# Kernel tuning notes

Measured on AMD Instinct MI355X. Metric: run time of the kernel, lower is better.

The kernel has to match this reference:

```python
import jax, jax.numpy as jnp
import numpy as np


def setup_inputs() -> dict:
    key = jax.random.key(0)
    k1, k2 = jax.random.split(key)
    B, T, D = 32, 2048, 1024
    query = jax.random.normal(k1, (B, D), dtype=jnp.float32)
    values = jax.random.normal(k2, (B, T, D), dtype=jnp.float32)
    return {"query": query, "values": values}


def reference(query, values):
    # score[b,t] = sum_d query[b,d] * values[b,t,d]
    score = jnp.einsum("bd,btd->bt", query, values)[..., None]  # [B,T,1]
    attention_weights = jax.nn.softmax(score, axis=1)           # [B,T,1]
    # context[b,d] = sum_t w[b,t] * values[b,t,d]
    context_vector = jnp.einsum("bt,btd->bd", attention_weights[..., 0], values)
    return (context_vector, attention_weights)
```

## Files before the change

kernel.cpp:

```cpp
#include <hip/hip_runtime.h>
#include <hip/hip_bf16.h>

#define BB 32
#define TT 2048
#define DD 1024
#define TCHUNK 32
#define NC (TT / TCHUNK)
#define WPB 4
#define BLOCKS_PER_B (NC / WPB)


__global__ __launch_bounds__(256) void attn_pass1(
    const float* __restrict__ query,
    const float* __restrict__ values,
    float* __restrict__ ws) {
    float* scores = ws;
    float* pm = ws + BB * TT;
    float* pl = pm + BB * NC;
    float* pctx = pl + BB * NC;

    const int tid  = threadIdx.x;
    const int lane = tid & 63;
    const int wave = tid >> 6;
    const int b     = blockIdx.x / BLOCKS_PER_B;
    const int chunk = (blockIdx.x % BLOCKS_PER_B) * WPB + wave;
    const int t0    = chunk * TCHUNK;

    const float4* qrow = (const float4*)(query + (size_t)b * DD);
    float qf[16];
#pragma unroll
    for (int g = 0; g < 4; g++) {
        float4 q4 = qrow[g * 64 + lane];
        qf[4 * g + 0] = q4.x; qf[4 * g + 1] = q4.y;
        qf[4 * g + 2] = q4.z; qf[4 * g + 3] = q4.w;
    }

    const float4* vbase = (const float4*)(values + ((size_t)b * TT + t0) * DD);

    float m = -INFINITY, l = 0.f;
    float ctx[16];
#pragma unroll
    for (int k = 0; k < 16; k++) ctx[k] = 0.f;

    float4 cur0[4], cur1[4];
#pragma unroll
    for (int g = 0; g < 4; g++) {
        cur0[g] = vbase[g * 64 + lane];
        cur1[g] = vbase[256 + g * 64 + lane];
    }

    for (int r = 0; r < TCHUNK; r += 2) {
        float4 nxt0[4], nxt1[4];
        const bool have_next = (r + 2 < TCHUNK);
        if (have_next) {
#pragma unroll
            for (int g = 0; g < 4; g++) {
                nxt0[g] = vbase[(size_t)(r + 2) * 256 + g * 64 + lane];
                nxt1[g] = vbase[(size_t)(r + 3) * 256 + g * 64 + lane];
            }
        }
        float vf0[16], vf1[16];
#pragma unroll
        for (int g = 0; g < 4; g++) {
            vf0[4 * g + 0] = cur0[g].x; vf0[4 * g + 1] = cur0[g].y;
            vf0[4 * g + 2] = cur0[g].z; vf0[4 * g + 3] = cur0[g].w;
            vf1[4 * g + 0] = cur1[g].x; vf1[4 * g + 1] = cur1[g].y;
            vf1[4 * g + 2] = cur1[g].z; vf1[4 * g + 3] = cur1[g].w;
        }

        float s0 = 0.f, s1 = 0.f;
#pragma unroll
        for (int k = 0; k < 16; k++) {
            s0 = fmaf(qf[k], vf0[k], s0);
            s1 = fmaf(qf[k], vf1[k], s1);
        }
#pragma unroll
        for (int off = 32; off >= 1; off >>= 1) {
            s0 += __shfl_xor(s0, off, 64);
            s1 += __shfl_xor(s1, off, 64);
        }

        if (s0 <= m) {
            float p = __expf(s0 - m);
            l += p;
#pragma unroll
            for (int k = 0; k < 16; k++) ctx[k] = fmaf(p, vf0[k], ctx[k]);
        } else {
            float corr = __expf(m - s0);
            m = s0;
            l = fmaf(l, corr, 1.f);
#pragma unroll
            for (int k = 0; k < 16; k++) ctx[k] = fmaf(ctx[k], corr, vf0[k]);
        }
        if (s1 <= m) {
            float p = __expf(s1 - m);
            l += p;
#pragma unroll
            for (int k = 0; k < 16; k++) ctx[k] = fmaf(p, vf1[k], ctx[k]);
        } else {
            float corr = __expf(m - s1);
            m = s1;
            l = fmaf(l, corr, 1.f);
#pragma unroll
            for (int k = 0; k < 16; k++) ctx[k] = fmaf(ctx[k], corr, vf1[k]);
        }

        if (lane == 0) {
            float2* sp = (float2*)(scores + (size_t)b * TT + t0 + r);
            *sp = make_float2(s0, s1);
        }
        if (have_next) {
#pragma unroll
            for (int g = 0; g < 4; g++) { cur0[g] = nxt0[g]; cur1[g] = nxt1[g]; }
        }
    }

    const int ci = b * NC + chunk;
    if (lane == 0) { pm[ci] = m; pl[ci] = l; }
    float4* pc = (float4*)(pctx + (size_t)ci * DD);
#pragma unroll
    for (int g = 0; g < 4; g++)
        pc[g * 64 + lane] = make_float4(ctx[4 * g + 0], ctx[4 * g + 1],
                                        ctx[4 * g + 2], ctx[4 * g + 3]);
}

__global__ __launch_bounds__(256) void attn_pass2(
    const float* __restrict__ ws,
    float* __restrict__ out) {
    const float* scores = ws;
    const float* pm = ws + BB * TT;
    const float* pl = pm + BB * NC;
    const float* pctx = pl + BB * NC;

    const int tid   = threadIdx.x;
    const int b     = blockIdx.x >> 2;
    const int slice = blockIdx.x & 3;

    __shared__ float s_e[NC];
    __shared__ float s_M, s_L;
    if (tid < 64) {
        float mi = pm[b * NC + tid];
        float li = pl[b * NC + tid];
        float M = mi;
#pragma unroll
        for (int off = 32; off >= 1; off >>= 1) M = fmaxf(M, __shfl_xor(M, off, 64));
        float e  = __expf(mi - M);
        float lw = li * e;
#pragma unroll
        for (int off = 32; off >= 1; off >>= 1) lw += __shfl_xor(lw, off, 64);
        s_e[tid] = e;
        if (tid == 0) { s_M = M; s_L = lw; }
    }
    __syncthreads();
    const float M  = s_M;
    const float rL = 1.0f / s_L;

    const int d = slice * 256 + tid;
    const float* base = pctx + (size_t)b * NC * DD + d;
    float acc = 0.f;
#pragma unroll 8
    for (int i = 0; i < NC; i++) acc = fmaf(base[(size_t)i * DD], s_e[i], acc);
    out[(size_t)b * DD + d] = acc * rL;

    float* wout = out + BB * DD;
#pragma unroll
    for (int k = 0; k < 2; k++) {
        int t = slice * 512 + k * 256 + tid;
        float w = __expf(scores[(size_t)b * TT + t] - M) * rL;
        wout[(size_t)b * TT + t] = w;
    }
}

extern "C" void kernel_launch(void* const* d_in, const int* in_sizes, int n_in,
                              void* d_out, int out_size, void* d_ws, size_t ws_size,
                              hipStream_t stream) {
    const float* query  = (const float*)d_in[0];
    const float* values = (const float*)d_in[1];
    float* ws = (float*)d_ws;
    float* out = (float*)d_out;

    attn_pass1<<<dim3(BB * BLOCKS_PER_B), dim3(256), 0, stream>>>(query, values, ws);
    attn_pass2<<<dim3(BB * 4), dim3(256), 0, stream>>>(ws, out);
}
```

Measured before the change: 367.7 us.

## Fuse softmax combine pass into main kernel via last-block atomic counter

Each block first merges its four waves' partial max, sum and context in LDS, so it writes one partial per block instead of one per wave. The second kernel is removed; the last block to finish each batch row, found with an atomic counter, does the final cross-block reduction and writes the normalized weights. This removes one kernel launch and cuts partial-context traffic by four. In exchange it adds a memset launch, thread fences, 16KB of LDS per block, and a serial tail done by 32 single blocks.

```diff
diff --git a/kernel.cpp b/kernel.cpp
--- a/kernel.cpp
+++ b/kernel.cpp
@@ -8,22 +8,30 @@
 #define NC (TT / TCHUNK)
 #define WPB 4
 #define BLOCKS_PER_B (NC / WPB)
-
-
-__global__ __launch_bounds__(256) void attn_pass1(
+#define NBLK BLOCKS_PER_B
+
+#define WS_PM   (BB * TT)
+#define WS_PL   (WS_PM + BB * NBLK)
+#define WS_PCTX (WS_PL + BB * NBLK)
+#define WS_CNT  (WS_PCTX + BB * NBLK * DD)
+
+__global__ __launch_bounds__(256) void attn_fused(
     const float* __restrict__ query,
     const float* __restrict__ values,
-    float* __restrict__ ws) {
+    float* __restrict__ ws,
+    float* __restrict__ out) {
     float* scores = ws;
-    float* pm = ws + BB * TT;
-    float* pl = pm + BB * NC;
-    float* pctx = pl + BB * NC;
+    float* pm   = ws + WS_PM;
+    float* pl   = ws + WS_PL;
+    float* pctx = ws + WS_PCTX;
+    int*   cnt  = (int*)(ws + WS_CNT);
 
     const int tid  = threadIdx.x;
     const int lane = tid & 63;
     const int wave = tid >> 6;
     const int b     = blockIdx.x / BLOCKS_PER_B;
-    const int chunk = (blockIdx.x % BLOCKS_PER_B) * WPB + wave;
+    const int blkin = blockIdx.x % BLOCKS_PER_B;
+    const int chunk = blkin * WPB + wave;
     const int t0    = chunk * TCHUNK;
 
     const float4* qrow = (const float4*)(query + (size_t)b * DD);
@@ -115,59 +123,84 @@
         }
     }
 
-    const int ci = b * NC + chunk;
-    if (lane == 0) { pm[ci] = m; pl[ci] = l; }
-    float4* pc = (float4*)(pctx + (size_t)ci * DD);
+    __shared__ float lds_ctx[WPB][DD];
+    __shared__ float lds_m[WPB], lds_l[WPB];
+    __shared__ int   s_last;
+
+    float4* lw = (float4*)lds_ctx[wave];
 #pragma unroll
     for (int g = 0; g < 4; g++)
-        pc[g * 64 + lane] = make_float4(ctx[4 * g + 0], ctx[4 * g + 1],
+        lw[g * 64 + lane] = make_float4(ctx[4 * g + 0], ctx[4 * g + 1],
                                         ctx[4 * g + 2], ctx[4 * g + 3]);
-}
-
-__global__ __launch_bounds__(256) void attn_pass2(
-    const float* __restrict__ ws,
-    float* __restrict__ out) {
-    const float* scores = ws;
-    const float* pm = ws + BB * TT;
-    const float* pl = pm + BB * NC;
-    const float* pctx = pl + BB * NC;
-
-    const int tid   = threadIdx.x;
-    const int b     = blockIdx.x >> 2;
-    const int slice = blockIdx.x & 3;
-
-    __shared__ float s_e[NC];
-    __shared__ float s_M, s_L;
+    if (lane == 0) { lds_m[wave] = m; lds_l[wave] = l; }
+    __syncthreads();
+
+    const float m0 = lds_m[0], m1 = lds_m[1], m2 = lds_m[2], m3 = lds_m[3];
+    const float mB = fmaxf(fmaxf(m0, m1), fmaxf(m2, m3));
+    const float e0 = __expf(m0 - mB), e1 = __expf(m1 - mB);
+    const float e2 = __expf(m2 - mB), e3 = __expf(m3 - mB);
+    const float lB = lds_l[0] * e0 + lds_l[1] * e1 + lds_l[2] * e2 + lds_l[3] * e3;
+
+    const int bc = b * NBLK + blkin;
+    {
+        float4 a = ((const float4*)lds_ctx[0])[tid];
+        float4 c = ((const float4*)lds_ctx[1])[tid];
+        float4 d = ((const float4*)lds_ctx[2])[tid];
+        float4 e = ((const float4*)lds_ctx[3])[tid];
+        float4 o;
+        o.x = fmaf(a.x, e0, fmaf(c.x, e1, fmaf(d.x, e2, e.x * e3)));
+        o.y = fmaf(a.y, e0, fmaf(c.y, e1, fmaf(d.y, e2, e.y * e3)));
+        o.z = fmaf(a.z, e0, fmaf(c.z, e1, fmaf(d.z, e2, e.z * e3)));
+        o.w = fmaf(a.w, e0, fmaf(c.w, e1, fmaf(d.w, e2, e.w * e3)));
+        ((float4*)(pctx + (size_t)bc * DD))[tid] = o;
+    }
+    if (tid == 0) { pm[bc] = mB; pl[bc] = lB; }
+
+    __threadfence();
+    __syncthreads();
+    if (tid == 0) s_last = (atomicAdd(&cnt[b], 1) == NBLK - 1);
+    __syncthreads();
+    if (!s_last) return;
+    __threadfence();
+
+    __shared__ float s_e16[NBLK];
+    __shared__ float s_M, s_rL;
     if (tid < 64) {
-        float mi = pm[b * NC + tid];
-        float li = pl[b * NC + tid];
+        float mi = (tid < NBLK) ? pm[b * NBLK + tid] : -INFINITY;
+        float li = (tid < NBLK) ? pl[b * NBLK + tid] : 0.f;
         float M = mi;
 #pragma unroll
         for (int off = 32; off >= 1; off >>= 1) M = fmaxf(M, __shfl_xor(M, off, 64));
         float e  = __expf(mi - M);
-        float lw = li * e;
-#pragma unroll
-        for (int off = 32; off >= 1; off >>= 1) lw += __shfl_xor(lw, off, 64);
-        s_e[tid] = e;
-        if (tid == 0) { s_M = M; s_L = lw; }
+        float lw2 = li * e;
+#pragma unroll
+        for (int off = 32; off >= 1; off >>= 1) lw2 += __shfl_xor(lw2, off, 64);
+        if (tid < NBLK) s_e16[tid] = e;
+        if (tid == 0) { s_M = M; s_rL = 1.0f / lw2; }
     }
     __syncthreads();
     const float M  = s_M;
-    const float rL = 1.0f / s_L;
-
-    const int d = slice * 256 + tid;
-    const float* base = pctx + (size_t)b * NC * DD + d;
-    float acc = 0.f;
-#pragma unroll 8
-    for (int i = 0; i < NC; i++) acc = fmaf(base[(size_t)i * DD], s_e[i], acc);
-    out[(size_t)b * DD + d] = acc * rL;
+    const float rL = s_rL;
+
+    {
+        const float4* base = (const float4*)(pctx + (size_t)b * NBLK * DD);
+        float4 acc = make_float4(0.f, 0.f, 0.f, 0.f);
+#pragma unroll
+        for (int i = 0; i < NBLK; i++) {
+            float4 p = base[i * (DD / 4) + tid];
+            float e = s_e16[i];
+            acc.x = fmaf(p.x, e, acc.x); acc.y = fmaf(p.y, e, acc.y);
+            acc.z = fmaf(p.z, e, acc.z); acc.w = fmaf(p.w, e, acc.w);
+        }
+        acc.x *= rL; acc.y *= rL; acc.z *= rL; acc.w *= rL;
+        ((float4*)(out + (size_t)b * DD))[tid] = acc;
+    }
 
     float* wout = out + BB * DD;
 #pragma unroll
-    for (int k = 0; k < 2; k++) {
-        int t = slice * 512 + k * 256 + tid;
-        float w = __expf(scores[(size_t)b * TT + t] - M) * rL;
-        wout[(size_t)b * TT + t] = w;
+    for (int k = 0; k < 8; k++) {
+        int t = k * 256 + tid;
+        wout[(size_t)b * TT + t] = __expf(scores[(size_t)b * TT + t] - M) * rL;
     }
 }
 
@@ -179,6 +212,6 @@
     float* ws = (float*)d_ws;
     float* out = (float*)d_out;
 
-    attn_pass1<<<dim3(BB * BLOCKS_PER_B), dim3(256), 0, stream>>>(query, values, ws);
-    attn_pass2<<<dim3(BB * 4), dim3(256), 0, stream>>>(ws, out);
+    hipMemsetAsync(ws + WS_CNT, 0, BB * sizeof(int), stream);
+    attn_fused<<<dim3(BB * BLOCKS_PER_B), dim3(256), 0, stream>>>(query, values, ws, out);
 }
```

New measurement: 431.5 us. +17.4%, slower.

## Shrink per-wave time chunks and merge wave partials in LDS per block

Applied to the files above, without the earlier changes.

Cuts each wave's time chunk from 32 to 8 rows, which quadruples the pass-1 grid to raise occupancy and memory-level parallelism on the bandwidth-bound read of values. To keep the number of partials pass 2 must combine at 64 per batch, the four waves in a block now merge their online-softmax states (max, sum, context) through shared memory before one block-level partial is written. A 4-blocks-per-SM launch bound is also added. The cost is a block barrier plus extra LDS traffic and 16 KB of shared memory per block, and each wave now does less work per launch.

```diff
diff --git a/kernel.cpp b/kernel.cpp
--- a/kernel.cpp
+++ b/kernel.cpp
@@ -4,26 +4,31 @@
 #define BB 32
 #define TT 2048
 #define DD 1024
-#define TCHUNK 32
+#define TCHUNK 8
 #define NC (TT / TCHUNK)
 #define WPB 4
 #define BLOCKS_PER_B (NC / WPB)
-
-
-__global__ __launch_bounds__(256) void attn_pass1(
+#define NBLK BLOCKS_PER_B
+
+#define WS_PM   (BB * TT)
+#define WS_PL   (WS_PM + BB * NBLK)
+#define WS_PCTX (WS_PL + BB * NBLK)
+
+__global__ __launch_bounds__(256, 4) void attn_pass1(
     const float* __restrict__ query,
     const float* __restrict__ values,
     float* __restrict__ ws) {
     float* scores = ws;
-    float* pm = ws + BB * TT;
-    float* pl = pm + BB * NC;
-    float* pctx = pl + BB * NC;
+    float* pm   = ws + WS_PM;
+    float* pl   = ws + WS_PL;
+    float* pctx = ws + WS_PCTX;
 
     const int tid  = threadIdx.x;
     const int lane = tid & 63;
     const int wave = tid >> 6;
     const int b     = blockIdx.x / BLOCKS_PER_B;
-    const int chunk = (blockIdx.x % BLOCKS_PER_B) * WPB + wave;
+    const int blkin = blockIdx.x % BLOCKS_PER_B;
+    const int chunk = blkin * WPB + wave;
     const int t0    = chunk * TCHUNK;
 
     const float4* qrow = (const float4*)(query + (size_t)b * DD);
@@ -115,32 +120,56 @@
         }
     }
 
-    const int ci = b * NC + chunk;
-    if (lane == 0) { pm[ci] = m; pl[ci] = l; }
-    float4* pc = (float4*)(pctx + (size_t)ci * DD);
+    __shared__ float lds_ctx[WPB][DD];
+    __shared__ float lds_m[WPB], lds_l[WPB];
+
+    float4* lw = (float4*)lds_ctx[wave];
 #pragma unroll
     for (int g = 0; g < 4; g++)
-        pc[g * 64 + lane] = make_float4(ctx[4 * g + 0], ctx[4 * g + 1],
+        lw[g * 64 + lane] = make_float4(ctx[4 * g + 0], ctx[4 * g + 1],
                                         ctx[4 * g + 2], ctx[4 * g + 3]);
+    if (lane == 0) { lds_m[wave] = m; lds_l[wave] = l; }
+    __syncthreads();
+
+    const float m0 = lds_m[0], m1 = lds_m[1], m2 = lds_m[2], m3 = lds_m[3];
+    const float mB = fmaxf(fmaxf(m0, m1), fmaxf(m2, m3));
+    const float e0 = __expf(m0 - mB), e1 = __expf(m1 - mB);
+    const float e2 = __expf(m2 - mB), e3 = __expf(m3 - mB);
+    const float lB = lds_l[0] * e0 + lds_l[1] * e1 + lds_l[2] * e2 + lds_l[3] * e3;
+
+    const int bc = b * NBLK + blkin;
+    {
+        float4 a = ((const float4*)lds_ctx[0])[tid];
+        float4 c = ((const float4*)lds_ctx[1])[tid];
+        float4 d = ((const float4*)lds_ctx[2])[tid];
+        float4 e = ((const float4*)lds_ctx[3])[tid];
+        float4 o;
+        o.x = fmaf(a.x, e0, fmaf(c.x, e1, fmaf(d.x, e2, e.x * e3)));
+        o.y = fmaf(a.y, e0, fmaf(c.y, e1, fmaf(d.y, e2, e.y * e3)));
+        o.z = fmaf(a.z, e0, fmaf(c.z, e1, fmaf(d.z, e2, e.z * e3)));
+        o.w = fmaf(a.w, e0, fmaf(c.w, e1, fmaf(d.w, e2, e.w * e3)));
+        ((float4*)(pctx + (size_t)bc * DD))[tid] = o;
+    }
+    if (tid == 0) { pm[bc] = mB; pl[bc] = lB; }
 }
 
 __global__ __launch_bounds__(256) void attn_pass2(
     const float* __restrict__ ws,
     float* __restrict__ out) {
     const float* scores = ws;
-    const float* pm = ws + BB * TT;
-    const float* pl = pm + BB * NC;
-    const float* pctx = pl + BB * NC;
+    const float* pm   = ws + WS_PM;
+    const float* pl   = ws + WS_PL;
+    const float* pctx = ws + WS_PCTX;
 
     const int tid   = threadIdx.x;
     const int b     = blockIdx.x >> 2;
     const int slice = blockIdx.x & 3;
 
-    __shared__ float s_e[NC];
+    __shared__ float s_e[NBLK];
     __shared__ float s_M, s_L;
     if (tid < 64) {
-        float mi = pm[b * NC + tid];
-        float li = pl[b * NC + tid];
+        float mi = pm[b * NBLK + tid];
+        float li = pl[b * NBLK + tid];
         float M = mi;
 #pragma unroll
         for (int off = 32; off >= 1; off >>= 1) M = fmaxf(M, __shfl_xor(M, off, 64));
@@ -156,10 +185,10 @@
     const float rL = 1.0f / s_L;
 
     const int d = slice * 256 + tid;
-    const float* base = pctx + (size_t)b * NC * DD + d;
+    const float* base = pctx + (size_t)b * NBLK * DD + d;
     float acc = 0.f;
 #pragma unroll 8
-    for (int i = 0; i < NC; i++) acc = fmaf(base[(size_t)i * DD], s_e[i], acc);
+    for (int i = 0; i < NBLK; i++) acc = fmaf(base[(size_t)i * DD], s_e[i], acc);
     out[(size_t)b * DD + d] = acc * rL;
 
     float* wout = out + BB * DD;
```

Result: no change. 372.3 us (+1.2%).
